# Kernel optimization log

Measured on AMD Instinct MI355X. Metric: run time of the kernel, lower is better.

The kernel has to match this reference:

```python
import jax, jax.numpy as jnp
import numpy as np

B, T, D, H = 4, 2048, 1024, 16
HS = D // H
EPS = 1e-5

def layer_norm(x, g, b):
    mu = jnp.mean(x, axis=-1, keepdims=True)
    var = jnp.var(x, axis=-1, keepdims=True)
    return (x - mu) * jax.lax.rsqrt(var + EPS) * g + b

def setup_inputs() -> dict:
    key = jax.random.key(0)
    ks = jax.random.split(key, 12)
    s_in = 1.0 / np.sqrt(D)
    s_ff = 1.0 / np.sqrt(4 * D)
    return {
        "x": jax.random.normal(ks[0], (B, T, D), jnp.float32),
        "Wq": jax.random.uniform(ks[1], (H, D, HS), jnp.float32, -s_in, s_in),
        "Wk": jax.random.uniform(ks[2], (H, D, HS), jnp.float32, -s_in, s_in),
        "Wv": jax.random.uniform(ks[3], (H, D, HS), jnp.float32, -s_in, s_in),
        "Wp": jax.random.uniform(ks[4], (D, D), jnp.float32, -s_in, s_in),
        "bp": jax.random.uniform(ks[5], (D,), jnp.float32, -s_in, s_in),
        "W1": jax.random.uniform(ks[6], (D, 4 * D), jnp.float32, -s_in, s_in),
        "b1": jax.random.uniform(ks[7], (4 * D,), jnp.float32, -s_in, s_in),
        "W2": jax.random.uniform(ks[8], (4 * D, D), jnp.float32, -s_ff, s_ff),
        "b2": jax.random.uniform(ks[9], (D,), jnp.float32, -s_ff, s_ff),
        "g1": jnp.ones((D,), jnp.float32),
        "be1": jnp.zeros((D,), jnp.float32),
        "g2": jnp.ones((D,), jnp.float32),
        "be2": jnp.zeros((D,), jnp.float32),
    }

def reference(x, Wq, Wk, Wv, Wp, bp, W1, b1, W2, b2, g1, be1, g2, be2):
    # pre-LN (note: residual uses the NORMALIZED tensor, matching original code)
    h = layer_norm(x, g1, be1)                          # [B,T,D]
    q = jnp.einsum('btd,hdk->bhtk', h, Wq)              # [B,H,T,hs]
    k = jnp.einsum('btd,hdk->bhtk', h, Wk)
    v = jnp.einsum('btd,hdk->bhtk', h, Wv)
    # NOTE: original scales by embedding_size**-0.5, not head_size
    scores = jnp.einsum('bhtk,bhsk->bhts', q, k) * (D ** -0.5)
    causal = jnp.tril(jnp.ones((T, T), bool))
    scores = jnp.where(causal, scores, -jnp.inf)
    att = jax.nn.softmax(scores, axis=-1)               # [B,H,T,T]
    o = jnp.einsum('bhts,bhsk->bhtk', att, v)
    o = o.transpose(0, 2, 1, 3).reshape(B, T, D)        # concat heads
    o = o @ Wp + bp
    x2 = h + o
    h2 = layer_norm(x2, g2, be2)
    ff = jax.nn.relu(h2 @ W1 + b1) @ W2 + b2
    return h2 + ff
```

## Files before the change

### kernel.cpp

```cpp
#include <hip/hip_runtime.h>
#include <hip/hip_bf16.h>

#define Bq 4
#define Tq 2048
#define Dq 1024
#define Hq 16
#define HSq 64
#define EPSq 1e-5f

typedef __attribute__((ext_vector_type(8))) short s16x8;
typedef __attribute__((ext_vector_type(4))) float f32x4;

#define GLL16(g, l)                                                        \
    __builtin_amdgcn_global_load_lds(                                      \
        (const __attribute__((address_space(1))) void*)(g),                \
        (__attribute__((address_space(3))) void*)(l), 16, 0, 0)

#define PH_BAR() do { __builtin_amdgcn_sched_barrier(0);                   \
                      __builtin_amdgcn_s_barrier();                        \
                      __builtin_amdgcn_sched_barrier(0); } while (0)

__device__ __forceinline__ ushort f2bf(float f) {
    union { float f; unsigned u; } x; x.f = f;
    unsigned r = x.u + 0x7fffu + ((x.u >> 16) & 1u);
    return (ushort)(r >> 16);
}

__global__ __launch_bounds__(256) void ln_bf16(const float* __restrict__ x,
                                               const float* __restrict__ g,
                                               const float* __restrict__ bb,
                                               float* __restrict__ y,
                                               ushort* __restrict__ y16) {
    __shared__ float sdata[8];
    int row = blockIdx.x;
    const float4* xr = (const float4*)(x + (size_t)row * Dq);
    float4 v = xr[threadIdx.x];
    float s  = v.x + v.y + v.z + v.w;
    float ss = v.x*v.x + v.y*v.y + v.z*v.z + v.w*v.w;
    for (int off = 32; off; off >>= 1) {
        s  += __shfl_down(s,  off);
        ss += __shfl_down(ss, off);
    }
    int lane = threadIdx.x & 63, wid = threadIdx.x >> 6;
    if (lane == 0) { sdata[wid] = s; sdata[4 + wid] = ss; }
    __syncthreads();
    if (threadIdx.x == 0) {
        sdata[0] = sdata[0] + sdata[1] + sdata[2] + sdata[3];
        sdata[4] = sdata[4] + sdata[5] + sdata[6] + sdata[7];
    }
    __syncthreads();
    float mu  = sdata[0] * (1.f / Dq);
    float var = sdata[4] * (1.f / Dq) - mu * mu;
    float inv = rsqrtf(var + EPSq);
    float4 gv = ((const float4*)g)[threadIdx.x];
    float4 bv = ((const float4*)bb)[threadIdx.x];
    float4 o;
    o.x = (v.x - mu) * inv * gv.x + bv.x;
    o.y = (v.y - mu) * inv * gv.y + bv.y;
    o.z = (v.z - mu) * inv * gv.z + bv.z;
    o.w = (v.w - mu) * inv * gv.w + bv.w;
    ((float4*)(y + (size_t)row * Dq))[threadIdx.x] = o;
    ushort4 u4;
    u4.x = f2bf(o.x); u4.y = f2bf(o.y); u4.z = f2bf(o.z); u4.w = f2bf(o.w);
    *(ushort4*)(y16 + (size_t)row * Dq + threadIdx.x * 4) = u4;
}

__global__ __launch_bounds__(256) void repack_qkvT(const float* __restrict__ Wqm,
                                                   const float* __restrict__ Wkm,
                                                   const float* __restrict__ Wvm,
                                                   ushort* __restrict__ out) {
    __shared__ float tile[64][65];
    int bid = blockIdx.x;
    int p  = bid >> 8;
    int hh = (bid >> 4) & 15;
    int kt = bid & 15;
    int k0 = kt * 64;
    const float* W = (p == 0) ? Wqm : ((p == 1) ? Wkm : Wvm);
    float scale = (p == 0) ? 0.03125f : 1.0f;
    int j  = threadIdx.x & 63;
    int i0 = threadIdx.x >> 6;
#pragma unroll
    for (int r = 0; r < 16; r++) {
        int i = r * 4 + i0;
        tile[i][j] = W[(size_t)hh * (Dq * HSq) + (size_t)(k0 + i) * HSq + j];
    }
    __syncthreads();
#pragma unroll
    for (int r = 0; r < 16; r++) {
        int i = r * 4 + i0;
        out[(size_t)(p * Dq + hh * HSq + i) * Dq + k0 + j] = f2bf(tile[j][i] * scale);
    }
}

__global__ __launch_bounds__(256) void transpose_cvt(const float* __restrict__ in,
                                                     ushort* __restrict__ out,
                                                     int K, int N) {
    __shared__ float tile[64][65];
    int k0 = blockIdx.y * 64, n0 = blockIdx.x * 64;
    int j  = threadIdx.x & 63;
    int i0 = threadIdx.x >> 6;
#pragma unroll
    for (int r = 0; r < 16; r++) {
        int i = r * 4 + i0;
        tile[i][j] = in[(size_t)(k0 + i) * N + n0 + j];
    }
    __syncthreads();
#pragma unroll
    for (int r = 0; r < 16; r++) {
        int i = r * 4 + i0;
        out[(size_t)(n0 + i) * K + k0 + j] = f2bf(tile[j][i]);
    }
}

__global__ __launch_bounds__(512, 2) void gemm_mp(const ushort* __restrict__ A,
                                                  const ushort* __restrict__ BT,
                                                  const float* __restrict__ bias,
                                                  const float* __restrict__ resid,
                                                  void* __restrict__ Cp,
                                                  ushort* __restrict__ vtg,
                                                  int M, int N, int K,
                                                  int lda, int ldc,
                                                  int relu, int out_bf16) {
    __shared__ ushort lds[2 * 8192 + 3 * 16384];
    ushort* Alds = lds;
    ushort* Blds = lds + 2 * 8192;

    int tid = threadIdx.x;
    int w = tid >> 6, lane = tid & 63;
    int lm = lane & 15, quad = lane >> 4;
    int wm = w >> 2, wn = w & 3;

    int nwg = gridDim.x;
    int bid = blockIdx.x;
    int wk = bid;
    if ((nwg & 7) == 0) { int cpx = nwg >> 3; wk = (bid & 7) * cpx + (bid >> 3); }
    int mtiles = M >> 7;
    int rt = wk % mtiles, ct = wk / mtiles;
    int row0 = rt << 7, col0 = ct << 8;

    int cswz = (lane & 7) ^ (lane >> 3);
    int srow = w * 8 + (lane >> 3);
    const ushort* pA = A  + (size_t)(row0 + srow) * lda + cswz * 8;
    const ushort* pB = BT + (size_t)(col0 + srow) * K  + cswz * 8;

    auto stageA = [&](int slot, int t) {
        const ushort* g = pA + (size_t)t * 64;
        ushort* l = Alds + slot * 8192 + w * 512;
        GLL16(g, l);
        GLL16(g + (size_t)64 * lda, l + 4096);
    };
    auto stageB = [&](int slot, int t, int h) {
        const ushort* g = pB + (size_t)t * 64 + (size_t)(h * 128) * K;
        ushort* l = Blds + slot * 16384 + h * 8192 + w * 512;
        GLL16(g, l);
        GLL16(g + (size_t)64 * K, l + 4096);
    };

    int swq0 = (quad * 8) ^ ((lm & 7) << 3);
    int swq1 = (32 + quad * 8) ^ ((lm & 7) << 3);

    f32x4 zero = {0.f, 0.f, 0.f, 0.f};
    f32x4 acc[4][4];
#pragma unroll
    for (int i = 0; i < 4; i++)
#pragma unroll
        for (int jj = 0; jj < 4; jj++) acc[i][jj] = zero;

    int nkt = K >> 6;

    stageA(0, 0);
    stageB(0, 0, 0); stageB(0, 0, 1);
    stageB(1, 1, 0); stageB(1, 1, 1);
    __builtin_amdgcn_sched_barrier(0);
    asm volatile("s_waitcnt vmcnt(4)" ::: "memory");
    __builtin_amdgcn_s_barrier();
    __builtin_amdgcn_sched_barrier(0);

    int sA = 0, sB = 0;
    for (int t = 0; t < nkt; ++t) {
        const bool stA = (t + 1 < nkt);
        const bool stB = (t + 2 < nkt);
        int sB2 = sB + 2; if (sB2 >= 3) sB2 -= 3;
        const ushort* Ab = Alds + sA * 8192  + (wm * 64 + lm) * 64;
        const ushort* Bb = Blds + sB * 16384 + (wn * 64 + lm) * 64;
        s16x8 a[4][2], b0[2][2], b1[2][2];

#pragma unroll
        for (int m = 0; m < 4; m++) {
            a[m][0] = *(const s16x8*)(Ab + m * 1024 + swq0);
            a[m][1] = *(const s16x8*)(Ab + m * 1024 + swq1);
        }
#pragma unroll
        for (int nf = 0; nf < 2; nf++) {
            b0[nf][0] = *(const s16x8*)(Bb + nf * 1024 + swq0);
            b0[nf][1] = *(const s16x8*)(Bb + nf * 1024 + swq1);
        }
        if (stA) stageA(sA ^ 1, t + 1);
        if (stB) stageB(sB2, t + 2, 0);
        PH_BAR();
        __builtin_amdgcn_s_setprio(1);
#pragma unroll
        for (int m = 0; m < 4; m++)
#pragma unroll
            for (int nf = 0; nf < 2; nf++) {
                f32x4 tt = __builtin_amdgcn_mfma_f32_16x16x32_bf16(a[m][0], b0[nf][0], acc[m][nf], 0, 0, 0);
                acc[m][nf] = __builtin_amdgcn_mfma_f32_16x16x32_bf16(a[m][1], b0[nf][1], tt, 0, 0, 0);
            }
        __builtin_amdgcn_s_setprio(0);
        PH_BAR();

#pragma unroll
        for (int nf = 0; nf < 2; nf++) {
            b1[nf][0] = *(const s16x8*)(Bb + (nf + 2) * 1024 + swq0);
            b1[nf][1] = *(const s16x8*)(Bb + (nf + 2) * 1024 + swq1);
        }
        if (stB) stageB(sB2, t + 2, 1);
        PH_BAR();
        __builtin_amdgcn_s_setprio(1);
#pragma unroll
        for (int m = 0; m < 4; m++)
#pragma unroll
            for (int nf = 0; nf < 2; nf++) {
                f32x4 tt = __builtin_amdgcn_mfma_f32_16x16x32_bf16(a[m][0], b1[nf][0], acc[m][nf + 2], 0, 0, 0);
                acc[m][nf + 2] = __builtin_amdgcn_mfma_f32_16x16x32_bf16(a[m][1], b1[nf][1], tt, 0, 0, 0);
            }
        __builtin_amdgcn_s_setprio(0);
        __builtin_amdgcn_sched_barrier(0);
        if (stB)      { asm volatile("s_waitcnt vmcnt(4)" ::: "memory"); }
        else if (stA) { asm volatile("s_waitcnt vmcnt(0)" ::: "memory"); }
        __builtin_amdgcn_s_barrier();
        __builtin_amdgcn_sched_barrier(0);

        sA ^= 1;
        sB += 1; if (sB >= 3) sB -= 3;
    }

    if (vtg && col0 >= 2048) {
#pragma unroll
        for (int m = 0; m < 4; m++) {
            int r0 = row0 + wm * 64 + m * 16 + quad * 4;
            int bb = r0 >> 11;
            int t  = r0 & (Tq - 1);
#pragma unroll
            for (int nf = 0; nf < 4; nf++) {
                int hsg = col0 - 2048 + wn * 64 + nf * 16 + lm;
                ushort4 u;
                u.x = f2bf(acc[m][nf][0]);
                u.y = f2bf(acc[m][nf][1]);
                u.z = f2bf(acc[m][nf][2]);
                u.w = f2bf(acc[m][nf][3]);
                *(ushort4*)(vtg + ((size_t)(bb * Hq + (hsg >> 6)) * HSq + (hsg & 63)) * Tq + t) = u;
            }
        }
        return;
    }

    float bcol[4];
#pragma unroll
    for (int nf = 0; nf < 4; nf++)
        bcol[nf] = bias ? bias[col0 + wn * 64 + nf * 16 + lm] : 0.f;

#pragma unroll
    for (int m = 0; m < 4; m++) {
#pragma unroll
        for (int p = 0; p < 4; p++) {
            int r = row0 + wm * 64 + m * 16 + quad * 4 + p;
#pragma unroll
            for (int nf = 0; nf < 4; nf++) {
                int c = col0 + wn * 64 + nf * 16 + lm;
                float v = acc[m][nf][p] + bcol[nf];
                if (relu) v = fmaxf(v, 0.f);
                if (resid) v += resid[(size_t)r * ldc + c];
                if (out_bf16) ((ushort*)Cp)[(size_t)r * ldc + c] = f2bf(v);
                else          ((float*)Cp)[(size_t)r * ldc + c] = v;
            }
        }
    }
}

__global__ __launch_bounds__(256) void attn_mfma(const ushort* __restrict__ qkv,
                                                 const ushort* __restrict__ VtG,
                                                 ushort* __restrict__ o16) {
    __shared__ ushort Ks[64 * 72];
    __shared__ ushort Vt[64 * 64];
    __shared__ ushort Ps[4 * 16 * 72];

    int gid = blockIdx.x;
    int b  = gid >> 8;
    int hh = (gid >> 4) & 15;
    int pr = (gid + 7 * b) & 15;
    int qa = pr;
    int qb = 31 - pr;

    int tid = threadIdx.x;
    int w = tid >> 6, lane = tid & 63;
    int lm = lane & 15, quad = lane >> 4;

    const int rs3 = 3 * Dq;
    const ushort* qbase = qkv + (size_t)(b * Tq) * rs3 + hh * HSq;
    int qra = qa * 64 + w * 16 + lm;
    int qrb = qb * 64 + w * 16 + lm;
    s16x8 aqa0 = *(const s16x8*)(qbase + (size_t)qra * rs3 + quad * 8);
    s16x8 aqa1 = *(const s16x8*)(qbase + (size_t)qra * rs3 + 32 + quad * 8);
    s16x8 aqb0 = *(const s16x8*)(qbase + (size_t)qrb * rs3 + quad * 8);
    s16x8 aqb1 = *(const s16x8*)(qbase + (size_t)qrb * rs3 + 32 + quad * 8);

    s16x8 ones;
#pragma unroll
    for (int j = 0; j < 8; j++) ones[j] = (short)0x3F80;

    f32x4 zero = {0.f, 0.f, 0.f, 0.f};
    f32x4 oa[4], ob[4];
#pragma unroll
    for (int nt = 0; nt < 4; nt++) { oa[nt] = zero; ob[nt] = zero; }
    f32x4 la = zero, lb = zero;

    const ushort* kbase = qkv + (size_t)(b * Tq) * rs3 + Dq + hh * HSq;
    const ushort* vtb = VtG + (size_t)((b * Hq + hh) * HSq) * Tq;

    int kr = tid >> 3, kc = (tid & 7) * 8;
    int vh = tid >> 2, vc0 = (tid & 3) * 8;
    int vswz = (((vh >> 3) ^ vh) & 7) << 3;

    s16x8 kp0 = *(const s16x8*)(kbase + (size_t)kr * rs3 + kc);
    s16x8 kp1 = *(const s16x8*)(kbase + (size_t)(kr + 32) * rs3 + kc);
    s16x8 vp0 = *(const s16x8*)(vtb + (size_t)vh * Tq + vc0);
    s16x8 vp1 = *(const s16x8*)(vtb + (size_t)vh * Tq + vc0 + 32);

    auto do_tile = [&](const s16x8& aq0, const s16x8& aq1,
                       f32x4 (&o_acc)[4], f32x4& l_acc, int diag) {
        f32x4 sacc[4];
#pragma unroll
        for (int kt2 = 0; kt2 < 4; kt2++) {
            const ushort* krp = &Ks[(kt2 * 16 + lm) * 72 + quad * 8];
            s16x8 bk0 = *(const s16x8*)krp;
            s16x8 bk1 = *(const s16x8*)(krp + 32);
            f32x4 t = __builtin_amdgcn_mfma_f32_16x16x32_bf16(aq0, bk0, zero, 0, 0, 0);
            sacc[kt2] = __builtin_amdgcn_mfma_f32_16x16x32_bf16(aq1, bk1, t, 0, 0, 0);
        }
        if (diag) {
#pragma unroll
            for (int kt2 = 0; kt2 < 4; kt2++)
#pragma unroll
                for (int r = 0; r < 4; r++)
                    if (kt2 * 16 + lm > w * 16 + quad * 4 + r) sacc[kt2][r] = -1e30f;
        }
#pragma unroll
        for (int kt2 = 0; kt2 < 4; kt2++)
#pragma unroll
            for (int r = 0; r < 4; r++)
                Ps[(w * 16 + quad * 4 + r) * 72 + kt2 * 16 + lm] = f2bf(__expf(sacc[kt2][r]));

        s16x8 ap0 = *(const s16x8*)&Ps[(w * 16 + lm) * 72 + quad * 8];
        s16x8 ap1 = *(const s16x8*)&Ps[(w * 16 + lm) * 72 + 32 + quad * 8];

#pragma unroll
        for (int nt = 0; nt < 4; nt++) {
            int n = nt * 16 + lm;
            int swz = (((n >> 3) ^ n) & 7) << 3;
            s16x8 bv0 = *(const s16x8*)&Vt[n * 64 + ((quad * 8) ^ swz)];
            s16x8 bv1 = *(const s16x8*)&Vt[n * 64 + ((32 + quad * 8) ^ swz)];
            f32x4 t = __builtin_amdgcn_mfma_f32_16x16x32_bf16(ap0, bv0, o_acc[nt], 0, 0, 0);
            o_acc[nt] = __builtin_amdgcn_mfma_f32_16x16x32_bf16(ap1, bv1, t, 0, 0, 0);
        }
        f32x4 t2 = __builtin_amdgcn_mfma_f32_16x16x32_bf16(ap0, ones, l_acc, 0, 0, 0);
        l_acc = __builtin_amdgcn_mfma_f32_16x16x32_bf16(ap1, ones, t2, 0, 0, 0);
    };

    for (int kt = 0; kt <= qb; kt++) {
        __syncthreads();
        *(s16x8*)&Ks[kr * 72 + kc] = kp0;
        *(s16x8*)&Ks[(kr + 32) * 72 + kc] = kp1;
        *(s16x8*)&Vt[vh * 64 + (vc0 ^ vswz)] = vp0;
        *(s16x8*)&Vt[vh * 64 + ((vc0 + 32) ^ vswz)] = vp1;
        __syncthreads();

        if (kt < qb) {
            const ushort* kb = kbase + (size_t)((kt + 1) * 64) * rs3;
            kp0 = *(const s16x8*)(kb + (size_t)kr * rs3 + kc);
            kp1 = *(const s16x8*)(kb + (size_t)(kr + 32) * rs3 + kc);
            const ushort* vb = vtb + (size_t)vh * Tq + (kt + 1) * 64;
            vp0 = *(const s16x8*)(vb + vc0);
            vp1 = *(const s16x8*)(vb + vc0 + 32);
        }

        do_tile(aqb0, aqb1, ob, lb, kt == qb);
        if (kt <= qa)
            do_tile(aqa0, aqa1, oa, la, kt == qa);
    }

#pragma unroll
    for (int r = 0; r < 4; r++) {
        float inva = 1.f / la[r];
        float invb = 1.f / lb[r];
        size_t rowa = (size_t)(b * Tq + qa * 64 + w * 16 + quad * 4 + r);
        size_t rowb = (size_t)(b * Tq + qb * 64 + w * 16 + quad * 4 + r);
#pragma unroll
        for (int nt = 0; nt < 4; nt++) {
            o16[rowa * Dq + hh * HSq + nt * 16 + lm] = f2bf(oa[nt][r] * inva);
            o16[rowb * Dq + hh * HSq + nt * 16 + lm] = f2bf(ob[nt][r] * invb);
        }
    }
}

extern "C" void kernel_launch(void* const* d_in, const int* in_sizes, int n_in,
                              void* d_out, int out_size, void* d_ws, size_t ws_size,
                              hipStream_t stream) {
    const float* x   = (const float*)d_in[0];
    const float* Wq  = (const float*)d_in[1];
    const float* Wk  = (const float*)d_in[2];
    const float* Wv  = (const float*)d_in[3];
    const float* Wp  = (const float*)d_in[4];
    const float* bp  = (const float*)d_in[5];
    const float* W1  = (const float*)d_in[6];
    const float* b1  = (const float*)d_in[7];
    const float* W2  = (const float*)d_in[8];
    const float* b2  = (const float*)d_in[9];
    const float* g1  = (const float*)d_in[10];
    const float* be1 = (const float*)d_in[11];
    const float* g2  = (const float*)d_in[12];
    const float* be2 = (const float*)d_in[13];
    float* out = (float*)d_out;

    const size_t MB = 1u << 20;
    char* ws = (char*)d_ws;
    float*  slotA = (float*)(ws);
    ushort* qkv   = (ushort*)(ws + 32 * MB);
    float*  pbuf  = (float*)(ws + 32 * MB);
    ushort* u16   = (ushort*)(ws + 32 * MB);
    ushort* slotC = (ushort*)(ws + 96 * MB);
    ushort* WqkvT = (ushort*)(ws + 112 * MB);
    ushort* WpT   = (ushort*)(ws + 118 * MB);
    ushort* W1T   = (ushort*)(ws + 120 * MB);
    ushort* W2T   = (ushort*)(ws + 128 * MB);
    ushort* VtG   = (ushort*)(ws + 136 * MB);

    const int rows = Bq * Tq;

    hipLaunchKernelGGL(repack_qkvT, dim3(3 * 16 * 16), dim3(256), 0, stream, Wq, Wk, Wv, WqkvT);
    hipLaunchKernelGGL(transpose_cvt, dim3(Dq / 64, Dq / 64), dim3(256), 0, stream, Wp, WpT, Dq, Dq);
    hipLaunchKernelGGL(transpose_cvt, dim3(4 * Dq / 64, Dq / 64), dim3(256), 0, stream, W1, W1T, Dq, 4 * Dq);
    hipLaunchKernelGGL(transpose_cvt, dim3(Dq / 64, 4 * Dq / 64), dim3(256), 0, stream, W2, W2T, 4 * Dq, Dq);

    hipLaunchKernelGGL(ln_bf16, dim3(rows), dim3(256), 0, stream, x, g1, be1, slotA, slotC);
    hipLaunchKernelGGL(gemm_mp, dim3((rows / 128) * (3 * Dq / 256)), dim3(512), 0, stream,
                       slotC, WqkvT, (const float*)nullptr, (const float*)nullptr, (void*)qkv, VtG,
                       rows, 3 * Dq, Dq, Dq, 3 * Dq, 0, 1);
    hipLaunchKernelGGL(attn_mfma, dim3(Bq * Hq * 16), dim3(256), 0, stream, qkv, VtG, slotC);
    hipLaunchKernelGGL(gemm_mp, dim3((rows / 128) * (Dq / 256)), dim3(512), 0, stream,
                       slotC, WpT, bp, slotA, (void*)pbuf, (ushort*)nullptr,
                       rows, Dq, Dq, Dq, Dq, 0, 0);
    hipLaunchKernelGGL(ln_bf16, dim3(rows), dim3(256), 0, stream, pbuf, g2, be2, slotA, slotC);
    hipLaunchKernelGGL(gemm_mp, dim3((rows / 128) * (4 * Dq / 256)), dim3(512), 0, stream,
                       slotC, W1T, b1, (const float*)nullptr, (void*)u16, (ushort*)nullptr,
                       rows, 4 * Dq, Dq, Dq, 4 * Dq, 1, 1);
    hipLaunchKernelGGL(gemm_mp, dim3((rows / 128) * (Dq / 256)), dim3(512), 0, stream,
                       u16, W2T, b2, slotA, (void*)out, (ushort*)nullptr,
                       rows, Dq, 4 * Dq, 4 * Dq, Dq, 0, 0);
}
```

Before: 529.2 us.

## Add 256x256-tile eight-phase pipelined GEMM for QKV, FFN1 and FFN2

Adds a new GEMM kernel that computes 256x256 output tiles per 512-thread block, using 128 KB of LDS double-buffered across two K-steps. Each iteration is split into eight barrier-separated phases that interleave global-to-LDS loads with MFMA bursts, and raise wave priority during the MFMA sections. It also remaps block IDs across XCDs. The larger tile raises operand reuse per loaded byte, but it halves the grid (FFN2 gets only 128 blocks), doubles accumulator register pressure, and uses 128 KB of LDS, which limits occupancy.

```diff
diff --git a/kernel.cpp b/kernel.cpp
--- a/kernel.cpp
+++ b/kernel.cpp
@@ -112,6 +112,279 @@
     }
 }
 
+__global__ __launch_bounds__(512, 2) void gemm_8ph(const ushort* __restrict__ A,
+                                                   const ushort* __restrict__ BT,
+                                                   const float* __restrict__ bias,
+                                                   const float* __restrict__ resid,
+                                                   void* __restrict__ Cp,
+                                                   ushort* __restrict__ vtg,
+                                                   int M, int N, int K,
+                                                   int lda, int ldc,
+                                                   int relu, int out_bf16) {
+    __shared__ ushort lds[65536];
+    ushort* Al = lds;
+    ushort* Bl = lds + 32768;
+
+    int tid = threadIdx.x;
+    int w = tid >> 6, lane = tid & 63;
+    int lm = lane & 15, quad = lane >> 4;
+    int wm = w >> 2, wn = w & 3;
+
+    int nwg = gridDim.x, bid = blockIdx.x, wk = bid;
+    if ((nwg & 7) == 0) { int cpx = nwg >> 3; wk = (bid & 7) * cpx + (bid >> 3); }
+    int mtiles = M >> 8;
+    int rt = wk % mtiles, ct = wk / mtiles;
+    int row0 = rt << 8, col0 = ct << 8;
+
+    int cswz = (lane & 7) ^ (lane >> 3);
+    int srow = w * 8 + (lane >> 3);
+    const ushort* pA = A  + (size_t)(row0 + srow) * lda + cswz * 8;
+    const ushort* pB = BT + (size_t)(col0 + srow) * K  + cswz * 8;
+
+    auto stA = [&](int h, int t) {
+        const ushort* g = pA + (size_t)(h * 128) * lda + (size_t)t * 64;
+        ushort* l = Al + ((t & 1) * 2 + h) * 8192 + w * 512;
+        GLL16(g, l);
+        GLL16(g + (size_t)64 * lda, l + 4096);
+    };
+    auto stB = [&](int h, int t) {
+        const ushort* g = pB + (size_t)(h * 128) * K + (size_t)t * 64;
+        ushort* l = Bl + ((t & 1) * 2 + h) * 8192 + w * 512;
+        GLL16(g, l);
+        GLL16(g + (size_t)64 * K, l + 4096);
+    };
+
+    int swq0 = (quad * 8) ^ ((lm & 7) << 3);
+    int swq1 = (32 + quad * 8) ^ ((lm & 7) << 3);
+
+    const ushort* A0b = Al + wm * 8192 + lm * 64;
+    const ushort* A1b = Al + (2 + wm) * 8192 + lm * 64;
+    const ushort* B0b = Bl + (wn >> 1) * 8192 + ((wn & 1) * 64 + lm) * 64;
+    const ushort* B1b = Bl + (2 + (wn >> 1)) * 8192 + ((wn & 1) * 64 + lm) * 64;
+
+    f32x4 zero = {0.f, 0.f, 0.f, 0.f};
+    f32x4 acc[8][4];
+#pragma unroll
+    for (int i = 0; i < 8; i++)
+#pragma unroll
+        for (int jj = 0; jj < 4; jj++) acc[i][jj] = zero;
+
+    int nkt = K >> 6;
+    int T = nkt >> 1;
+
+    stB(0, 0); __builtin_amdgcn_sched_barrier(0);
+    stB(1, 0); __builtin_amdgcn_sched_barrier(0);
+    stA(0, 0); __builtin_amdgcn_sched_barrier(0);
+    stA(1, 0); __builtin_amdgcn_sched_barrier(0);
+    stB(0, 1); __builtin_amdgcn_sched_barrier(0);
+    stB(1, 1);
+    __builtin_amdgcn_sched_barrier(0);
+    asm volatile("s_waitcnt vmcnt(4)" ::: "memory");
+    __builtin_amdgcn_s_barrier();
+    __builtin_amdgcn_sched_barrier(0);
+
+    for (int j = 0; j < T; ++j) {
+        int o = 2 * j + 1, e2 = 2 * j + 2, o2 = 2 * j + 3;
+        const bool stg = (j + 1 < T);
+        s16x8 a[4][2], b[2][2], c[2][2];
+
+#pragma unroll
+        for (int m = 0; m < 4; m++) {
+            a[m][0] = *(const s16x8*)(A0b + m * 1024 + swq0);
+            a[m][1] = *(const s16x8*)(A0b + m * 1024 + swq1);
+        }
+#pragma unroll
+        for (int n = 0; n < 2; n++) {
+            b[n][0] = *(const s16x8*)(B0b + n * 1024 + swq0);
+            b[n][1] = *(const s16x8*)(B0b + n * 1024 + swq1);
+        }
+        stA(0, o);
+        PH_BAR();
+        __builtin_amdgcn_s_setprio(1);
+#pragma unroll
+        for (int m = 0; m < 4; m++)
+#pragma unroll
+            for (int n = 0; n < 2; n++) {
+                f32x4 t = __builtin_amdgcn_mfma_f32_16x16x32_bf16(a[m][0], b[n][0], acc[m][n], 0, 0, 0);
+                acc[m][n] = __builtin_amdgcn_mfma_f32_16x16x32_bf16(a[m][1], b[n][1], t, 0, 0, 0);
+            }
+        __builtin_amdgcn_s_setprio(0);
+        PH_BAR();
+
+#pragma unroll
+        for (int n = 0; n < 2; n++) {
+            c[n][0] = *(const s16x8*)(B0b + (n + 2) * 1024 + swq0);
+            c[n][1] = *(const s16x8*)(B0b + (n + 2) * 1024 + swq1);
+        }
+        stA(1, o);
+        PH_BAR();
+        __builtin_amdgcn_s_setprio(1);
+#pragma unroll
+        for (int m = 0; m < 4; m++)
+#pragma unroll
+            for (int n = 0; n < 2; n++) {
+                f32x4 t = __builtin_amdgcn_mfma_f32_16x16x32_bf16(a[m][0], c[n][0], acc[m][n + 2], 0, 0, 0);
+                acc[m][n + 2] = __builtin_amdgcn_mfma_f32_16x16x32_bf16(a[m][1], c[n][1], t, 0, 0, 0);
+            }
+        __builtin_amdgcn_s_setprio(0);
+        PH_BAR();
+
+#pragma unroll
+        for (int m = 0; m < 4; m++) {
+            a[m][0] = *(const s16x8*)(A0b + (m + 4) * 1024 + swq0);
+            a[m][1] = *(const s16x8*)(A0b + (m + 4) * 1024 + swq1);
+        }
+        if (stg) stB(0, e2);
+        PH_BAR();
+        __builtin_amdgcn_s_setprio(1);
+#pragma unroll
+        for (int m = 0; m < 4; m++)
+#pragma unroll
+            for (int n = 0; n < 2; n++) {
+                f32x4 t = __builtin_amdgcn_mfma_f32_16x16x32_bf16(a[m][0], b[n][0], acc[m + 4][n], 0, 0, 0);
+                acc[m + 4][n] = __builtin_amdgcn_mfma_f32_16x16x32_bf16(a[m][1], b[n][1], t, 0, 0, 0);
+            }
+        __builtin_amdgcn_s_setprio(0);
+        PH_BAR();
+
+        if (stg) stB(1, e2);
+        PH_BAR();
+        __builtin_amdgcn_s_setprio(1);
+#pragma unroll
+        for (int m = 0; m < 4; m++)
+#pragma unroll
+            for (int n = 0; n < 2; n++) {
+                f32x4 t = __builtin_amdgcn_mfma_f32_16x16x32_bf16(a[m][0], c[n][0], acc[m + 4][n + 2], 0, 0, 0);
+                acc[m + 4][n + 2] = __builtin_amdgcn_mfma_f32_16x16x32_bf16(a[m][1], c[n][1], t, 0, 0, 0);
+            }
+        __builtin_amdgcn_s_setprio(0);
+        __builtin_amdgcn_sched_barrier(0);
+        if (stg) { asm volatile("s_waitcnt vmcnt(4)" ::: "memory"); }
+        else     { asm volatile("s_waitcnt vmcnt(0)" ::: "memory"); }
+        __builtin_amdgcn_s_barrier();
+        __builtin_amdgcn_sched_barrier(0);
+
+#pragma unroll
+        for (int m = 0; m < 4; m++) {
+            a[m][0] = *(const s16x8*)(A1b + m * 1024 + swq0);
+            a[m][1] = *(const s16x8*)(A1b + m * 1024 + swq1);
+        }
+#pragma unroll
+        for (int n = 0; n < 2; n++) {
+            b[n][0] = *(const s16x8*)(B1b + n * 1024 + swq0);
+            b[n][1] = *(const s16x8*)(B1b + n * 1024 + swq1);
+        }
+        if (stg) stA(0, e2);
+        PH_BAR();
+        __builtin_amdgcn_s_setprio(1);
+#pragma unroll
+        for (int m = 0; m < 4; m++)
+#pragma unroll
+            for (int n = 0; n < 2; n++) {
+                f32x4 t = __builtin_amdgcn_mfma_f32_16x16x32_bf16(a[m][0], b[n][0], acc[m][n], 0, 0, 0);
+                acc[m][n] = __builtin_amdgcn_mfma_f32_16x16x32_bf16(a[m][1], b[n][1], t, 0, 0, 0);
+            }
+        __builtin_amdgcn_s_setprio(0);
+        PH_BAR();
+
+#pragma unroll
+        for (int n = 0; n < 2; n++) {
+            c[n][0] = *(const s16x8*)(B1b + (n + 2) * 1024 + swq0);
+            c[n][1] = *(const s16x8*)(B1b + (n + 2) * 1024 + swq1);
+        }
+        if (stg) stA(1, e2);
+        PH_BAR();
+        __builtin_amdgcn_s_setprio(1);
+#pragma unroll
+        for (int m = 0; m < 4; m++)
+#pragma unroll
+            for (int n = 0; n < 2; n++) {
+                f32x4 t = __builtin_amdgcn_mfma_f32_16x16x32_bf16(a[m][0], c[n][0], acc[m][n + 2], 0, 0, 0);
+                acc[m][n + 2] = __builtin_amdgcn_mfma_f32_16x16x32_bf16(a[m][1], c[n][1], t, 0, 0, 0);
+            }
+        __builtin_amdgcn_s_setprio(0);
+        PH_BAR();
+
+#pragma unroll
+        for (int m = 0; m < 4; m++) {
+            a[m][0] = *(const s16x8*)(A1b + (m + 4) * 1024 + swq0);
+            a[m][1] = *(const s16x8*)(A1b + (m + 4) * 1024 + swq1);
+        }
+        if (stg) stB(0, o2);
+        PH_BAR();
+        __builtin_amdgcn_s_setprio(1);
+#pragma unroll
+        for (int m = 0; m < 4; m++)
+#pragma unroll
+            for (int n = 0; n < 2; n++) {
+                f32x4 t = __builtin_amdgcn_mfma_f32_16x16x32_bf16(a[m][0], b[n][0], acc[m + 4][n], 0, 0, 0);
+                acc[m + 4][n] = __builtin_amdgcn_mfma_f32_16x16x32_bf16(a[m][1], b[n][1], t, 0, 0, 0);
+            }
+        __builtin_amdgcn_s_setprio(0);
+        PH_BAR();
+
+        if (stg) stB(1, o2);
+        PH_BAR();
+        __builtin_amdgcn_s_setprio(1);
+#pragma unroll
+        for (int m = 0; m < 4; m++)
+#pragma unroll
+            for (int n = 0; n < 2; n++) {
+                f32x4 t = __builtin_amdgcn_mfma_f32_16x16x32_bf16(a[m][0], c[n][0], acc[m + 4][n + 2], 0, 0, 0);
+                acc[m + 4][n + 2] = __builtin_amdgcn_mfma_f32_16x16x32_bf16(a[m][1], c[n][1], t, 0, 0, 0);
+            }
+        __builtin_amdgcn_s_setprio(0);
+        if (stg) {
+            __builtin_amdgcn_sched_barrier(0);
+            asm volatile("s_waitcnt vmcnt(4)" ::: "memory");
+            __builtin_amdgcn_s_barrier();
+            __builtin_amdgcn_sched_barrier(0);
+        }
+    }
+
+    if (vtg && col0 >= 2048) {
+#pragma unroll
+        for (int m = 0; m < 8; m++) {
+            int r0 = row0 + wm * 128 + m * 16 + quad * 4;
+            int bb = r0 >> 11;
+            int t  = r0 & (Tq - 1);
+#pragma unroll
+            for (int nf = 0; nf < 4; nf++) {
+                int hsg = col0 - 2048 + wn * 64 + nf * 16 + lm;
+                ushort4 u;
+                u.x = f2bf(acc[m][nf][0]);
+                u.y = f2bf(acc[m][nf][1]);
+                u.z = f2bf(acc[m][nf][2]);
+                u.w = f2bf(acc[m][nf][3]);
+                *(ushort4*)(vtg + ((size_t)(bb * Hq + (hsg >> 6)) * HSq + (hsg & 63)) * Tq + t) = u;
+            }
+        }
+        return;
+    }
+
+    float bcol[4];
+#pragma unroll
+    for (int nf = 0; nf < 4; nf++)
+        bcol[nf] = bias ? bias[col0 + wn * 64 + nf * 16 + lm] : 0.f;
+
+#pragma unroll
+    for (int m = 0; m < 8; m++) {
+#pragma unroll
+        for (int p = 0; p < 4; p++) {
+            int r = row0 + wm * 128 + m * 16 + quad * 4 + p;
+#pragma unroll
+            for (int nf = 0; nf < 4; nf++) {
+                int cc = col0 + wn * 64 + nf * 16 + lm;
+                float v = acc[m][nf][p] + bcol[nf];
+                if (relu) v = fmaxf(v, 0.f);
+                if (resid) v += resid[(size_t)r * ldc + cc];
+                if (out_bf16) ((ushort*)Cp)[(size_t)r * ldc + cc] = f2bf(v);
+                else          ((float*)Cp)[(size_t)r * ldc + cc] = v;
+            }
+        }
+    }
+}
+
 __global__ __launch_bounds__(512, 2) void gemm_mp(const ushort* __restrict__ A,
                                                   const ushort* __restrict__ BT,
                                                   const float* __restrict__ bias,
@@ -267,12 +540,12 @@
             int r = row0 + wm * 64 + m * 16 + quad * 4 + p;
 #pragma unroll
             for (int nf = 0; nf < 4; nf++) {
-                int c = col0 + wn * 64 + nf * 16 + lm;
+                int cc = col0 + wn * 64 + nf * 16 + lm;
                 float v = acc[m][nf][p] + bcol[nf];
                 if (relu) v = fmaxf(v, 0.f);
-                if (resid) v += resid[(size_t)r * ldc + c];
-                if (out_bf16) ((ushort*)Cp)[(size_t)r * ldc + c] = f2bf(v);
-                else          ((float*)Cp)[(size_t)r * ldc + c] = v;
+                if (resid) v += resid[(size_t)r * ldc + cc];
+                if (out_bf16) ((ushort*)Cp)[(size_t)r * ldc + cc] = f2bf(v);
+                else          ((float*)Cp)[(size_t)r * ldc + cc] = v;
             }
         }
     }
@@ -443,7 +716,7 @@
     hipLaunchKernelGGL(transpose_cvt, dim3(Dq / 64, 4 * Dq / 64), dim3(256), 0, stream, W2, W2T, 4 * Dq, Dq);
 
     hipLaunchKernelGGL(ln_bf16, dim3(rows), dim3(256), 0, stream, x, g1, be1, slotA, slotC);
-    hipLaunchKernelGGL(gemm_mp, dim3((rows / 128) * (3 * Dq / 256)), dim3(512), 0, stream,
+    hipLaunchKernelGGL(gemm_8ph, dim3((rows / 256) * (3 * Dq / 256)), dim3(512), 0, stream,
                        slotC, WqkvT, (const float*)nullptr, (const float*)nullptr, (void*)qkv, VtG,
                        rows, 3 * Dq, Dq, Dq, 3 * Dq, 0, 1);
     hipLaunchKernelGGL(attn_mfma, dim3(Bq * Hq * 16), dim3(256), 0, stream, qkv, VtG, slotC);
@@ -451,10 +724,10 @@
                        slotC, WpT, bp, slotA, (void*)pbuf, (ushort*)nullptr,
                        rows, Dq, Dq, Dq, Dq, 0, 0);
     hipLaunchKernelGGL(ln_bf16, dim3(rows), dim3(256), 0, stream, pbuf, g2, be2, slotA, slotC);
-    hipLaunchKernelGGL(gemm_mp, dim3((rows / 128) * (4 * Dq / 256)), dim3(512), 0, stream,
+    hipLaunchKernelGGL(gemm_8ph, dim3((rows / 256) * (4 * Dq / 256)), dim3(512), 0, stream,
                        slotC, W1T, b1, (const float*)nullptr, (void*)u16, (ushort*)nullptr,
                        rows, 4 * Dq, Dq, Dq, 4 * Dq, 1, 1);
-    hipLaunchKernelGGL(gemm_mp, dim3((rows / 128) * (Dq / 256)), dim3(512), 0, stream,
+    hipLaunchKernelGGL(gemm_8ph, dim3((rows / 256) * (Dq / 256)), dim3(512), 0, stream,
                        u16, W2T, b2, slotA, (void*)out, (ushort*)nullptr,
                        rows, Dq, 4 * Dq, 4 * Dq, Dq, 0, 0);
 }
```

New measurement: 551.4 us. +4.2%, slower.

## Shrink GEMM tile to 128x128 with 4 waves and single-phase B staging

Applied to the files above, without the earlier changes.

Replaces the 512-thread 128x256 GEMM with a 256-thread 128x128 variant: 4 waves in a 2x2 arrangement, B triple buffer halved, and each stage issuing four 32-row global-to-LDS loads. B for tile t+2 is now staged in one go in the second phase instead of split across both. The end-of-iteration barrier is skipped on the final iteration. The aim is more workgroups and smaller LDS use to improve occupancy and wave balance, at the cost of lower arithmetic reuse per tile, twice as many blocks, and unchanged vmcnt wait counts that now have to cover a different set of outstanding loads.

```diff
diff --git a/kernel.cpp b/kernel.cpp
--- a/kernel.cpp
+++ b/kernel.cpp
@@ -112,23 +112,23 @@
     }
 }
 
-__global__ __launch_bounds__(512, 2) void gemm_mp(const ushort* __restrict__ A,
-                                                  const ushort* __restrict__ BT,
-                                                  const float* __restrict__ bias,
-                                                  const float* __restrict__ resid,
-                                                  void* __restrict__ Cp,
-                                                  ushort* __restrict__ vtg,
-                                                  int M, int N, int K,
-                                                  int lda, int ldc,
-                                                  int relu, int out_bf16) {
-    __shared__ ushort lds[2 * 8192 + 3 * 16384];
+__global__ __launch_bounds__(256, 2) void gemm_bf16(const ushort* __restrict__ A,
+                                                    const ushort* __restrict__ BT,
+                                                    const float* __restrict__ bias,
+                                                    const float* __restrict__ resid,
+                                                    void* __restrict__ Cp,
+                                                    ushort* __restrict__ vtg,
+                                                    int M, int N, int K,
+                                                    int lda, int ldc,
+                                                    int relu, int out_bf16) {
+    __shared__ ushort lds[2 * 8192 + 3 * 8192];
     ushort* Alds = lds;
     ushort* Blds = lds + 2 * 8192;
 
     int tid = threadIdx.x;
     int w = tid >> 6, lane = tid & 63;
     int lm = lane & 15, quad = lane >> 4;
-    int wm = w >> 2, wn = w & 3;
+    int wm = w >> 1, wn = w & 1;
 
     int nwg = gridDim.x;
     int bid = blockIdx.x;
@@ -136,7 +136,7 @@
     if ((nwg & 7) == 0) { int cpx = nwg >> 3; wk = (bid & 7) * cpx + (bid >> 3); }
     int mtiles = M >> 7;
     int rt = wk % mtiles, ct = wk / mtiles;
-    int row0 = rt << 7, col0 = ct << 8;
+    int row0 = rt << 7, col0 = ct << 7;
 
     int cswz = (lane & 7) ^ (lane >> 3);
     int srow = w * 8 + (lane >> 3);
@@ -144,16 +144,16 @@
     const ushort* pB = BT + (size_t)(col0 + srow) * K  + cswz * 8;
 
     auto stageA = [&](int slot, int t) {
-        const ushort* g = pA + (size_t)t * 64;
-        ushort* l = Alds + slot * 8192 + w * 512;
-        GLL16(g, l);
-        GLL16(g + (size_t)64 * lda, l + 4096);
+#pragma unroll
+        for (int s = 0; s < 4; s++)
+            GLL16(pA + (size_t)t * 64 + (size_t)(s * 32) * lda,
+                  Alds + slot * 8192 + s * 2048 + w * 512);
     };
-    auto stageB = [&](int slot, int t, int h) {
-        const ushort* g = pB + (size_t)t * 64 + (size_t)(h * 128) * K;
-        ushort* l = Blds + slot * 16384 + h * 8192 + w * 512;
-        GLL16(g, l);
-        GLL16(g + (size_t)64 * K, l + 4096);
+    auto stageB = [&](int slot, int t) {
+#pragma unroll
+        for (int s = 0; s < 4; s++)
+            GLL16(pB + (size_t)t * 64 + (size_t)(s * 32) * K,
+                  Blds + slot * 8192 + s * 2048 + w * 512);
     };
 
     int swq0 = (quad * 8) ^ ((lm & 7) << 3);
@@ -169,8 +169,8 @@
     int nkt = K >> 6;
 
     stageA(0, 0);
-    stageB(0, 0, 0); stageB(0, 0, 1);
-    stageB(1, 1, 0); stageB(1, 1, 1);
+    stageB(0, 0);
+    stageB(1, 1);
     __builtin_amdgcn_sched_barrier(0);
     asm volatile("s_waitcnt vmcnt(4)" ::: "memory");
     __builtin_amdgcn_s_barrier();
@@ -181,8 +181,8 @@
         const bool stA = (t + 1 < nkt);
         const bool stB = (t + 2 < nkt);
         int sB2 = sB + 2; if (sB2 >= 3) sB2 -= 3;
-        const ushort* Ab = Alds + sA * 8192  + (wm * 64 + lm) * 64;
-        const ushort* Bb = Blds + sB * 16384 + (wn * 64 + lm) * 64;
+        const ushort* Ab = Alds + sA * 8192 + (wm * 64 + lm) * 64;
+        const ushort* Bb = Blds + sB * 8192 + (wn * 64 + lm) * 64;
         s16x8 a[4][2], b0[2][2], b1[2][2];
 
 #pragma unroll
@@ -196,7 +196,6 @@
             b0[nf][1] = *(const s16x8*)(Bb + nf * 1024 + swq1);
         }
         if (stA) stageA(sA ^ 1, t + 1);
-        if (stB) stageB(sB2, t + 2, 0);
         PH_BAR();
         __builtin_amdgcn_s_setprio(1);
 #pragma unroll
@@ -214,7 +213,7 @@
             b1[nf][0] = *(const s16x8*)(Bb + (nf + 2) * 1024 + swq0);
             b1[nf][1] = *(const s16x8*)(Bb + (nf + 2) * 1024 + swq1);
         }
-        if (stB) stageB(sB2, t + 2, 1);
+        if (stB) stageB(sB2, t + 2);
         PH_BAR();
         __builtin_amdgcn_s_setprio(1);
 #pragma unroll
@@ -228,8 +227,10 @@
         __builtin_amdgcn_sched_barrier(0);
         if (stB)      { asm volatile("s_waitcnt vmcnt(4)" ::: "memory"); }
         else if (stA) { asm volatile("s_waitcnt vmcnt(0)" ::: "memory"); }
-        __builtin_amdgcn_s_barrier();
-        __builtin_amdgcn_sched_barrier(0);
+        if (stA) {
+            __builtin_amdgcn_s_barrier();
+            __builtin_amdgcn_sched_barrier(0);
+        }
 
         sA ^= 1;
         sB += 1; if (sB >= 3) sB -= 3;
@@ -267,12 +268,12 @@
             int r = row0 + wm * 64 + m * 16 + quad * 4 + p;
 #pragma unroll
             for (int nf = 0; nf < 4; nf++) {
-                int c = col0 + wn * 64 + nf * 16 + lm;
+                int cc = col0 + wn * 64 + nf * 16 + lm;
                 float v = acc[m][nf][p] + bcol[nf];
                 if (relu) v = fmaxf(v, 0.f);
-                if (resid) v += resid[(size_t)r * ldc + c];
-                if (out_bf16) ((ushort*)Cp)[(size_t)r * ldc + c] = f2bf(v);
-                else          ((float*)Cp)[(size_t)r * ldc + c] = v;
+                if (resid) v += resid[(size_t)r * ldc + cc];
+                if (out_bf16) ((ushort*)Cp)[(size_t)r * ldc + cc] = f2bf(v);
+                else          ((float*)Cp)[(size_t)r * ldc + cc] = v;
             }
         }
     }
@@ -443,18 +444,18 @@
     hipLaunchKernelGGL(transpose_cvt, dim3(Dq / 64, 4 * Dq / 64), dim3(256), 0, stream, W2, W2T, 4 * Dq, Dq);
 
     hipLaunchKernelGGL(ln_bf16, dim3(rows), dim3(256), 0, stream, x, g1, be1, slotA, slotC);
-    hipLaunchKernelGGL(gemm_mp, dim3((rows / 128) * (3 * Dq / 256)), dim3(512), 0, stream,
+    hipLaunchKernelGGL(gemm_bf16, dim3((rows / 128) * (3 * Dq / 128)), dim3(256), 0, stream,
                        slotC, WqkvT, (const float*)nullptr, (const float*)nullptr, (void*)qkv, VtG,
                        rows, 3 * Dq, Dq, Dq, 3 * Dq, 0, 1);
     hipLaunchKernelGGL(attn_mfma, dim3(Bq * Hq * 16), dim3(256), 0, stream, qkv, VtG, slotC);
-    hipLaunchKernelGGL(gemm_mp, dim3((rows / 128) * (Dq / 256)), dim3(512), 0, stream,
+    hipLaunchKernelGGL(gemm_bf16, dim3((rows / 128) * (Dq / 128)), dim3(256), 0, stream,
                        slotC, WpT, bp, slotA, (void*)pbuf, (ushort*)nullptr,
                        rows, Dq, Dq, Dq, Dq, 0, 0);
     hipLaunchKernelGGL(ln_bf16, dim3(rows), dim3(256), 0, stream, pbuf, g2, be2, slotA, slotC);
-    hipLaunchKernelGGL(gemm_mp, dim3((rows / 128) * (4 * Dq / 256)), dim3(512), 0, stream,
+    hipLaunchKernelGGL(gemm_bf16, dim3((rows / 128) * (4 * Dq / 128)), dim3(256), 0, stream,
                        slotC, W1T, b1, (const float*)nullptr, (void*)u16, (ushort*)nullptr,
                        rows, 4 * Dq, Dq, Dq, 4 * Dq, 1, 1);
-    hipLaunchKernelGGL(gemm_mp, dim3((rows / 128) * (Dq / 256)), dim3(512), 0, stream,
+    hipLaunchKernelGGL(gemm_bf16, dim3((rows / 128) * (Dq / 128)), dim3(256), 0, stream,
                        u16, W2T, b2, slotA, (void*)out, (ushort*)nullptr,
                        rows, Dq, 4 * Dq, 4 * Dq, Dq, 0, 0);
 }
```

Result: slower. 544.8 us (+2.9%).
